# Performance work log

Measured on AMD Instinct MI355X. Metric: run time of the kernel, lower is better.

The kernel has to match this reference:

```python
import jax, jax.numpy as jnp
import numpy as np

B, G, P = 4096, 31, 8
C = P * (P + 1) // 2  # 36 pairwise-with-replacement combinations


def setup_inputs() -> dict:
    key = jax.random.key(0)
    k1, k2 = jax.random.split(key)
    param_tensor = jax.random.normal(k1, (B, G, G, P), dtype=jnp.float32)
    integral_coeffs = jax.random.normal(k2, (G, G, C), dtype=jnp.float32)
    return {"param_tensor": param_tensor, "integral_coeffs": integral_coeffs}


def reference(param_tensor, integral_coeffs):
    # torch.combinations(param, 2, with_replacement=True).prod(-1) over last dim
    # == param[ii] * param[jj] for upper-triangular-with-diagonal index pairs.
    P_ = param_tensor.shape[-1]
    ii, jj = np.triu_indices(P_)  # same ordering as torch.combinations with_replacement
    pairs = param_tensor[..., ii] * param_tensor[..., jj]  # [B, G, G, C]
    # weight by per-cell coeffs, sum over pair dim and over both grid dims -> [B]
    return jnp.einsum('bghc,ghc->b', pairs, integral_coeffs)
```

## Files before the change

### kernel.cpp

```cpp
#include <hip/hip_runtime.h>

#define B_  4096
#define G_  31
#define GG_ 961
#define P_  8
#define C_  36
#define R_  8

__global__ void zero_kernel(float* out, int n) {
    int i = blockIdx.x * blockDim.x + threadIdx.x;
    if (i < n) out[i] = 0.0f;
}

__global__ __launch_bounds__(256, 4)
void quadform_kernel(const float* __restrict__ param,
                     const float* __restrict__ coef,
                     float* __restrict__ out) {
    const int lane    = threadIdx.x & 63;
    const int wv      = threadIdx.x >> 6;
    const int gh_tile = blockIdx.x * 4 + wv;
    const int gh      = gh_tile * 64 + lane;
    const bool valid  = gh < GG_;
    const int  ghc    = valid ? gh : (GG_ - 1);

    float cf[C_];
    {
        const float4* cp = reinterpret_cast<const float4*>(coef) + (size_t)ghc * (C_ / 4);
        #pragma unroll
        for (int q = 0; q < C_ / 4; ++q) {
            float4 v = cp[q];
            cf[4*q+0] = v.x; cf[4*q+1] = v.y; cf[4*q+2] = v.z; cf[4*q+3] = v.w;
        }
    }
    if (!valid) {
        #pragma unroll
        for (int c = 0; c < C_; ++c) cf[c] = 0.0f;
    }

    const int b0 = blockIdx.y * R_;
    const float4* pb = reinterpret_cast<const float4*>(param);
    const size_t base = ((size_t)b0 * GG_ + ghc) * 2;
    const size_t bstep = (size_t)GG_ * 2;

    float4 qa[4][2], qb[4][2];
    #pragma unroll
    for (int r = 0; r < 4; ++r) {
        qa[r][0] = pb[base + (size_t)r * bstep];
        qa[r][1] = pb[base + (size_t)r * bstep + 1];
    }
    #pragma unroll
    for (int r = 0; r < 4; ++r) {
        qb[r][0] = pb[base + (size_t)(r + 4) * bstep];
        qb[r][1] = pb[base + (size_t)(r + 4) * bstep + 1];
    }

    float s[R_];
    #pragma unroll
    for (int h = 0; h < 2; ++h) {
        #pragma unroll
        for (int r = 0; r < 4; ++r) {
            float4 p0 = h ? qb[r][0] : qa[r][0];
            float4 p1 = h ? qb[r][1] : qa[r][1];
            const float pv[P_] = {p0.x, p0.y, p0.z, p0.w, p1.x, p1.y, p1.z, p1.w};
            float acc = 0.0f;
            int c = 0;
            #pragma unroll
            for (int i = 0; i < P_; ++i) {
                #pragma unroll
                for (int j = i; j < P_; ++j) {
                    acc = fmaf(cf[c] * pv[i], pv[j], acc);
                    ++c;
                }
            }
            s[h * 4 + r] = acc;
        }
    }

    #pragma unroll
    for (int off = 32; off; off >>= 1) {
        #pragma unroll
        for (int r = 0; r < R_; ++r) s[r] += __shfl_xor(s[r], off, 64);
    }

    if (lane == 0) {
        #pragma unroll
        for (int r = 0; r < R_; ++r) atomicAdd(&out[b0 + r], s[r]);
    }
}

extern "C" void kernel_launch(void* const* d_in, const int* in_sizes, int n_in,
                              void* d_out, int out_size, void* d_ws, size_t ws_size,
                              hipStream_t stream) {
    const float* param = (const float*)d_in[0];
    const float* coef  = (const float*)d_in[1];
    float* out = (float*)d_out;

    zero_kernel<<<(B_ + 255) / 256, 256, 0, stream>>>(out, B_);

    dim3 grid(4, B_ / R_);
    quadform_kernel<<<grid, 256, 0, stream>>>(param, coef, out);
}
```

Before: 184.0 us.

## Give each block whole batch rows to drop atomics and zero kernel

Result: slower. 321.8 us (+74.9%).

```diff
diff --git a/kernel.cpp b/kernel.cpp
--- a/kernel.cpp
+++ b/kernel.cpp
@@ -5,74 +5,69 @@
 #define GG_ 961
 #define P_  8
 #define C_  36
-#define R_  8
-
-__global__ void zero_kernel(float* out, int n) {
-    int i = blockIdx.x * blockDim.x + threadIdx.x;
-    if (i < n) out[i] = 0.0f;
-}
+#define R_  4
 
 __global__ __launch_bounds__(256, 4)
 void quadform_kernel(const float* __restrict__ param,
                      const float* __restrict__ coef,
                      float* __restrict__ out) {
-    const int lane    = threadIdx.x & 63;
-    const int wv      = threadIdx.x >> 6;
-    const int gh_tile = blockIdx.x * 4 + wv;
-    const int gh      = gh_tile * 64 + lane;
-    const bool valid  = gh < GG_;
-    const int  ghc    = valid ? gh : (GG_ - 1);
+    const int tid  = threadIdx.x;
+    const int lane = tid & 63;
+    const int wv   = tid >> 6;
+    const int b0   = blockIdx.x * R_;
 
-    float cf[C_];
-    {
-        const float4* cp = reinterpret_cast<const float4*>(coef) + (size_t)ghc * (C_ / 4);
-        #pragma unroll
-        for (int q = 0; q < C_ / 4; ++q) {
-            float4 v = cp[q];
-            cf[4*q+0] = v.x; cf[4*q+1] = v.y; cf[4*q+2] = v.z; cf[4*q+3] = v.w;
-        }
-    }
-    if (!valid) {
-        #pragma unroll
-        for (int c = 0; c < C_; ++c) cf[c] = 0.0f;
-    }
+    __shared__ float red[4][R_];
 
-    const int b0 = blockIdx.y * R_;
+    float s[R_] = {0.0f, 0.0f, 0.0f, 0.0f};
+
     const float4* pb = reinterpret_cast<const float4*>(param);
-    const size_t base = ((size_t)b0 * GG_ + ghc) * 2;
+    const float4* cb = reinterpret_cast<const float4*>(coef);
     const size_t bstep = (size_t)GG_ * 2;
 
-    float4 qa[4][2], qb[4][2];
-    #pragma unroll
-    for (int r = 0; r < 4; ++r) {
-        qa[r][0] = pb[base + (size_t)r * bstep];
-        qa[r][1] = pb[base + (size_t)r * bstep + 1];
-    }
-    #pragma unroll
-    for (int r = 0; r < 4; ++r) {
-        qb[r][0] = pb[base + (size_t)(r + 4) * bstep];
-        qb[r][1] = pb[base + (size_t)(r + 4) * bstep + 1];
-    }
+    for (int pass = 0; pass < 4; ++pass) {
+        const int  gh    = pass * 256 + tid;
+        const bool valid = gh < GG_;
+        const int  ghc   = valid ? gh : (GG_ - 1);
 
-    float s[R_];
-    #pragma unroll
-    for (int h = 0; h < 2; ++h) {
+        const size_t base = ((size_t)b0 * GG_ + ghc) * 2;
+        float4 p[R_][2];
         #pragma unroll
-        for (int r = 0; r < 4; ++r) {
-            float4 p0 = h ? qb[r][0] : qa[r][0];
-            float4 p1 = h ? qb[r][1] : qa[r][1];
-            const float pv[P_] = {p0.x, p0.y, p0.z, p0.w, p1.x, p1.y, p1.z, p1.w};
+        for (int r = 0; r < R_; ++r) {
+            p[r][0] = pb[base + (size_t)r * bstep];
+            p[r][1] = pb[base + (size_t)r * bstep + 1];
+        }
+
+        float cf[C_];
+        {
+            const float4* cp = cb + (size_t)ghc * (C_ / 4);
+            #pragma unroll
+            for (int q = 0; q < C_ / 4; ++q) {
+                float4 v = cp[q];
+                cf[4*q+0] = v.x; cf[4*q+1] = v.y; cf[4*q+2] = v.z; cf[4*q+3] = v.w;
+            }
+        }
+        if (!valid) {
+            #pragma unroll
+            for (int c = 0; c < C_; ++c) cf[c] = 0.0f;
+        }
+
+        #pragma unroll
+        for (int r = 0; r < R_; ++r) {
+            const float pv[P_] = {p[r][0].x, p[r][0].y, p[r][0].z, p[r][0].w,
+                                  p[r][1].x, p[r][1].y, p[r][1].z, p[r][1].w};
             float acc = 0.0f;
             int c = 0;
             #pragma unroll
             for (int i = 0; i < P_; ++i) {
+                float t = 0.0f;
                 #pragma unroll
                 for (int j = i; j < P_; ++j) {
-                    acc = fmaf(cf[c] * pv[i], pv[j], acc);
+                    t = fmaf(cf[c], pv[j], t);
                     ++c;
                 }
+                acc = fmaf(pv[i], t, acc);
             }
-            s[h * 4 + r] = acc;
+            s[r] += acc;
         }
     }
 
@@ -81,10 +76,14 @@
         #pragma unroll
         for (int r = 0; r < R_; ++r) s[r] += __shfl_xor(s[r], off, 64);
     }
-
     if (lane == 0) {
         #pragma unroll
-        for (int r = 0; r < R_; ++r) atomicAdd(&out[b0 + r], s[r]);
+        for (int r = 0; r < R_; ++r) red[wv][r] = s[r];
+    }
+    __syncthreads();
+
+    if (tid < R_) {
+        out[b0 + tid] = red[0][tid] + red[1][tid] + red[2][tid] + red[3][tid];
     }
 }
 
@@ -95,8 +94,5 @@
     const float* coef  = (const float*)d_in[1];
     float* out = (float*)d_out;
 
-    zero_kernel<<<(B_ + 255) / 256, 256, 0, stream>>>(out, B_);
-
-    dim3 grid(4, B_ / R_);
-    quadform_kernel<<<grid, 256, 0, stream>>>(param, coef, out);
+    quadform_kernel<<<B_ / R_, 256, 0, stream>>>(param, coef, out);
 }
```
